# Performance work log

Measured on AMD Instinct MI355X. Metric: run time of the kernel, lower is better.

Reference implementation:

```python
import jax, jax.numpy as jnp
import numpy as np

B, C, T, K = 16, 512, 2048, 64

def setup_inputs() -> dict:
    key = jax.random.key(0)
    k1, k2, k3 = jax.random.split(key, 3)
    v = jax.random.normal(k1, (B, C, T), dtype=jnp.float32)
    # 1x1 Conv1d weights == linear maps over channel dim
    Wk = jax.random.normal(k2, (K, C), dtype=jnp.float32) * 0.02
    bk = jnp.zeros((K,), dtype=jnp.float32)
    Wq = jax.random.normal(k3, (K, C), dtype=jnp.float32) * 0.02
    bq = jnp.zeros((K,), dtype=jnp.float32)
    gamma = jnp.ones((), dtype=jnp.float32)
    return {"v": v, "Wk": Wk, "bk": bk, "Wq": Wq, "bq": bq, "gamma": gamma}

def reference(v, Wk, bk, Wq, bq, gamma):
    # k, q: (B, K, T) via 1x1 conv = channel-wise linear
    k = jnp.einsum('kc,bct->bkt', Wk, v) + bk[None, :, None]
    q = jnp.einsum('kc,bct->bkt', Wq, v) + bq[None, :, None]
    # original: e1[b,d,i,j]=q[b,d,j], e2[b,d,i,j]=k[b,d,i]; sum over d
    # -> s[b,i,j] = sum_d k[b,d,i] * q[b,d,j]  (avoid materializing B,K,T,T)
    s = jnp.einsum('bdi,bdj->bij', k, q)  # (B, T, T)
    a = jax.nn.softmax(s, axis=1)          # softmax over dim=1 (the i axis)
    att = jnp.einsum('bct,btj->bcj', v, a)  # bmm(v, a)
    return v + gamma * att
```

## Files before the change

### kernel.cpp

```cpp
#include <hip/hip_runtime.h>

#define Bc 16
#define Cc 512
#define Tc 2048
#define QT 128
#define KT 128
#define NT 16
#define LTS 66

typedef __attribute__((ext_vector_type(8)))  short short8;
typedef __attribute__((ext_vector_type(4)))  float f32x4;
typedef __attribute__((ext_vector_type(16))) float f32x16;
typedef unsigned short u16;

static __device__ __forceinline__ u16 f2bf(float x) {
  unsigned u = __float_as_uint(x);
  u += 0x7FFF + ((u >> 16) & 1);
  return (u16)(u >> 16);
}

static __device__ __forceinline__ unsigned cvt_pk_bf16(float lo, float hi) {
  unsigned r;
  asm("v_cvt_pk_bf16_f32 %0, %1, %2" : "=v"(r) : "v"(lo), "v"(hi));
  return r;
}

static __device__ __forceinline__ void gload_lds16(const u16* gsrc, u16* ldst) {
  __builtin_amdgcn_global_load_lds(
      (const __attribute__((address_space(1))) unsigned int*)gsrc,
      (__attribute__((address_space(3))) unsigned int*)ldst,
      16, 0, 0);
}

static __device__ __forceinline__ void block_sync_lds() {
  __builtin_amdgcn_sched_barrier(0);
  asm volatile("s_waitcnt lgkmcnt(0)" ::: "memory");
  __builtin_amdgcn_s_barrier();
  __builtin_amdgcn_sched_barrier(0);
}

static __device__ __forceinline__ void block_sync_vm4() {
  __builtin_amdgcn_sched_barrier(0);
  asm volatile("s_waitcnt vmcnt(4) lgkmcnt(0)" ::: "memory");
  __builtin_amdgcn_s_barrier();
  __builtin_amdgcn_sched_barrier(0);
}

__global__ __launch_bounds__(256) void prep_kernel(
    const float* __restrict__ Wk, const float* __restrict__ Wq,
    const float* __restrict__ bk, const float* __restrict__ bq,
    u16* __restrict__ Wbf, float* __restrict__ bkq)
{
  int idx  = blockIdx.x * 256 + threadIdx.x;
  int base = idx * 4;
  if (base < 128 * Cc) {
    int ch = base >> 9;
    int c  = base & (Cc - 1);
    const float* src = (ch < 64) ? (Wk + (size_t)ch * Cc + c)
                                 : (Wq + (size_t)(ch - 64) * Cc + c);
    f32x4 w = *reinterpret_cast<const f32x4*>(src);
    uint2 o;
    o.x = (unsigned)f2bf(w[0]) | ((unsigned)f2bf(w[1]) << 16);
    o.y = (unsigned)f2bf(w[2]) | ((unsigned)f2bf(w[3]) << 16);
    *reinterpret_cast<uint2*>(Wbf + base) = o;
  }
  if (idx < 128) bkq[idx] = (idx < 64) ? bk[idx] : bq[idx - 64];
}

__global__ __launch_bounds__(256) void kqv_kernel(
    const float* __restrict__ v, const u16* __restrict__ Wbf,
    const float* __restrict__ bkq, u16* __restrict__ kq, u16* __restrict__ vbf)
{
  __shared__ u16 LDSt[2][64][LTS];
  const int b   = blockIdx.y;
  const int t0  = blockIdx.x * 64;
  const int tid = threadIdx.x;
  const int lane = tid & 63;
  const int w    = tid >> 6;
  const int l15  = lane & 15;
  const int lg   = lane >> 4;

  f32x4 acc[8];
  #pragma unroll
  for (int mt = 0; mt < 8; ++mt) acc[mt] = f32x4{0.f, 0.f, 0.f, 0.f};

  const float* vb = v + (size_t)b * Cc * Tc + t0;
  float x[16];
  #pragma unroll
  for (int r = 0; r < 16; ++r) x[r] = vb[(size_t)(w * 16 + r) * Tc + lane];

  int buf = 0;
  for (int c0 = 0; c0 < Cc; c0 += 64, buf ^= 1) {
    #pragma unroll
    for (int r = 0; r < 16; ++r) {
      u16 hb = f2bf(x[r]);
      LDSt[buf][lane][w * 16 + r] = hb;
      vbf[((size_t)b * Cc + c0 + w * 16 + r) * Tc + t0 + lane] = hb;
    }
    block_sync_lds();
    if (c0 + 64 < Cc) {
      #pragma unroll
      for (int r = 0; r < 16; ++r)
        x[r] = vb[(size_t)(c0 + 64 + w * 16 + r) * Tc + lane];
    }
    #pragma unroll
    for (int ks = 0; ks < 2; ++ks) {
      short8 bfrag = *reinterpret_cast<const short8*>(&LDSt[buf][w * 16 + l15][ks * 32 + lg * 8]);
      #pragma unroll
      for (int mt = 0; mt < 8; ++mt) {
        short8 afrag = *reinterpret_cast<const short8*>(
            Wbf + (size_t)(mt * 16 + l15) * Cc + c0 + ks * 32 + lg * 8);
        acc[mt] = __builtin_amdgcn_mfma_f32_16x16x32_bf16(afrag, bfrag, acc[mt], 0, 0, 0);
      }
    }
  }
  const int t = t0 + w * 16 + l15;
  u16* op = kq + ((size_t)b * Tc + t) * 128;
  #pragma unroll
  for (int mt = 0; mt < 8; ++mt) {
    int chb = mt * 16 + lg * 4;
    uint2 o;
    o.x = cvt_pk_bf16(acc[mt][0] + bkq[chb + 0], acc[mt][1] + bkq[chb + 1]);
    o.y = cvt_pk_bf16(acc[mt][2] + bkq[chb + 2], acc[mt][3] + bkq[chb + 3]);
    *reinterpret_cast<uint2*>(op + chb) = o;
  }
}

#define VLOAD(VF, KSB, IB)                                                \
  _Pragma("unroll")                                                       \
  for (int ct_ = 0; ct_ < 2; ++ct_)                                       \
    _Pragma("unroll")                                                     \
    for (int kk_ = 0; kk_ < 2; ++kk_)                                     \
      VF[ct_][kk_] = *reinterpret_cast<const short8*>(                    \
          vbase + (size_t)(ct_ * 32 + l31) * Tc + (IB) + ((KSB) + kk_) * 16 + kh * 8);

#define PVSTEP(VF, KSB)                                                   \
  {                                                                       \
    _Pragma("unroll")                                                     \
    for (int kk_ = 0; kk_ < 2; ++kk_) {                                   \
      short8 pf_[4];                                                      \
      _Pragma("unroll")                                                   \
      for (int jt_ = 0; jt_ < 4; ++jt_) {                                 \
        int row_ = jt_ * 32 + l31;                                        \
        int chk_ = ((((KSB) + kk_) * 2 + kh) ^ (row_ & 15)) * 8;          \
        pf_[jt_] = *reinterpret_cast<const short8*>(&P[pb][row_ * 128 + chk_]); \
      }                                                                   \
      _Pragma("unroll")                                                   \
      for (int jt_ = 0; jt_ < 4; ++jt_) {                                 \
        O32[0][jt_] = __builtin_amdgcn_mfma_f32_32x32x16_bf16(VF[0][kk_], pf_[jt_], O32[0][jt_], 0, 0, 0); \
        O32[1][jt_] = __builtin_amdgcn_mfma_f32_32x32x16_bf16(VF[1][kk_], pf_[jt_], O32[1][jt_], 0, 0, 0); \
      }                                                                   \
    }                                                                     \
  }

__global__ __launch_bounds__(512, 2) void attn_kernel(
    const float* __restrict__ v, const u16* __restrict__ vbf,
    const u16* __restrict__ kq, const float* __restrict__ gamma_p,
    float* __restrict__ out)
{
  __shared__ u16 P[2][128 * 128];
  __shared__ u16 Klds[2][128 * 64];
  __shared__ float lsum_lds[QT];
  __shared__ __align__(16) float linv_lds[QT];

  const int L   = blockIdx.x;
  const int lin = (L & 7) * 32 + (L >> 3);
  const int b   = lin >> 4;
  const int j0  = (lin & 15) * QT;
  const int tid = threadIdx.x;
  const int lane = tid & 63;
  const int wid  = tid >> 6;
  const int l15  = lane & 15;
  const int lg   = lane >> 4;
  const int l31  = lane & 31;
  const int kh   = lane >> 5;
  const int c0   = wid * 64;

  const int sc = (lane & 7) ^ ((lane >> 3) & 7);
  const u16* kqb2 = kq + (size_t)b * Tc * 128;
  u16* kst = &Klds[0][0] + wid * 16 * 64;

  short8 qf0, qf1;
  {
    const u16* qp = kq + (size_t)(b * Tc + j0 + wid * 16 + l15) * 128 + 64 + lg * 8;
    qf0 = *reinterpret_cast<const short8*>(qp);
    qf1 = *reinterpret_cast<const short8*>(qp + 32);
  }

  f32x16 O32[2][4];
  #pragma unroll
  for (int a = 0; a < 2; ++a)
    #pragma unroll
    for (int bb = 0; bb < 4; ++bb)
      #pragma unroll
      for (int e = 0; e < 16; ++e) O32[a][bb][e] = 0.f;

  float lsum = 0.f;

  const u16* vbase = vbf + ((size_t)b * Cc + c0) * Tc;
  short8 vfA[2][2], vfB[2][2];

  gload_lds16(kqb2 + (size_t)(wid * 16 + (lane >> 3)) * 128 + sc * 8, kst);
  gload_lds16(kqb2 + (size_t)(wid * 16 + 8 + (lane >> 3)) * 128 + sc * 8, kst + 8 * 64);
  __syncthreads();
  {
    u16* prow = &P[0][(wid * 16 + l15) * 128];
    #pragma unroll
    for (int hg = 0; hg < 2; ++hg) {
      short8 kf[4][2];
      #pragma unroll
      for (int it2 = 0; it2 < 4; ++it2)
        #pragma unroll
        for (int ks = 0; ks < 2; ++ks)
          kf[it2][ks] = *reinterpret_cast<const short8*>(
              &Klds[0][((hg * 4 + it2) * 16 + l15) * 64 + (((ks * 4 + lg) ^ (l15 & 7)) * 8)]);
      f32x4 sacc[4];
      #pragma unroll
      for (int it2 = 0; it2 < 4; ++it2) {
        f32x4 s = f32x4{0.f, 0.f, 0.f, 0.f};
        s = __builtin_amdgcn_mfma_f32_16x16x32_bf16(kf[it2][0], qf0, s, 0, 0, 0);
        s = __builtin_amdgcn_mfma_f32_16x16x32_bf16(kf[it2][1], qf1, s, 0, 0, 0);
        sacc[it2] = s;
      }
      #pragma unroll
      for (int it2 = 0; it2 < 4; ++it2) {
        float p0 = __expf(sacc[it2][0]);
        float p1 = __expf(sacc[it2][1]);
        float p2 = __expf(sacc[it2][2]);
        float p3 = __expf(sacc[it2][3]);
        lsum += (p0 + p1) + (p2 + p3);
        uint2 wv;
        wv.x = cvt_pk_bf16(p0, p1);
        wv.y = cvt_pk_bf16(p2, p3);
        int chk = ((hg * 8 + it2 * 2 + (lg >> 1)) ^ (l15 & 15)) * 8 + (lg & 1) * 4;
        *reinterpret_cast<uint2*>(prow + chk) = wv;
      }
    }
  }
  gload_lds16(kqb2 + (size_t)(KT + wid * 16 + (lane >> 3)) * 128 + sc * 8, kst + 8192);
  gload_lds16(kqb2 + (size_t)(KT + wid * 16 + 8 + (lane >> 3)) * 128 + sc * 8, kst + 8192 + 8 * 64);
  VLOAD(vfA, 0, 0);
  block_sync_vm4();

  int pb = 0;
  for (int i = 0; i < NT; ++i, pb ^= 1) {
    const int i0 = i * KT;
    const bool last = (i + 1 >= NT);

    VLOAD(vfB, 2, i0);

    if (i + 2 < NT) {
      const size_t kb = (size_t)(i0 + 2 * KT);
      gload_lds16(kqb2 + (kb + wid * 16 + (lane >> 3)) * 128 + sc * 8,
                  kst + (i & 1) * 8192);
      gload_lds16(kqb2 + (kb + wid * 16 + 8 + (lane >> 3)) * 128 + sc * 8,
                  kst + (i & 1) * 8192 + 8 * 64);
    }

    if (!last) {
      const u16* kl = &Klds[(i + 1) & 1][0];
      u16* prow = &P[pb ^ 1][(wid * 16 + l15) * 128];
      #pragma unroll
      for (int hg = 0; hg < 2; ++hg) {
        short8 kf[4][2];
        #pragma unroll
        for (int it2 = 0; it2 < 4; ++it2)
          #pragma unroll
          for (int ks = 0; ks < 2; ++ks)
            kf[it2][ks] = *reinterpret_cast<const short8*>(
                &kl[((hg * 4 + it2) * 16 + l15) * 64 + (((ks * 4 + lg) ^ (l15 & 7)) * 8)]);
        f32x4 sacc[4];
        #pragma unroll
        for (int it2 = 0; it2 < 4; ++it2) {
          f32x4 s = f32x4{0.f, 0.f, 0.f, 0.f};
          s = __builtin_amdgcn_mfma_f32_16x16x32_bf16(kf[it2][0], qf0, s, 0, 0, 0);
          s = __builtin_amdgcn_mfma_f32_16x16x32_bf16(kf[it2][1], qf1, s, 0, 0, 0);
          sacc[it2] = s;
        }
        #pragma unroll
        for (int it2 = 0; it2 < 4; ++it2) {
          float p0 = __expf(sacc[it2][0]);
          float p1 = __expf(sacc[it2][1]);
          float p2 = __expf(sacc[it2][2]);
          float p3 = __expf(sacc[it2][3]);
          lsum += (p0 + p1) + (p2 + p3);
          uint2 wv;
          wv.x = cvt_pk_bf16(p0, p1);
          wv.y = cvt_pk_bf16(p2, p3);
          int chk = ((hg * 8 + it2 * 2 + (lg >> 1)) ^ (l15 & 15)) * 8 + (lg & 1) * 4;
          *reinterpret_cast<uint2*>(prow + chk) = wv;
        }
      }
    }

    PVSTEP(vfA, 0);
    VLOAD(vfA, 4, i0);
    PVSTEP(vfB, 2);
    VLOAD(vfB, 6, i0);
    PVSTEP(vfA, 4);
    if (!last) VLOAD(vfA, 0, i0 + KT);
    PVSTEP(vfB, 6);

    if (!last) block_sync_vm4();
  }

  lsum += __shfl_xor(lsum, 16);
  lsum += __shfl_xor(lsum, 32);
  if (lane < 16) lsum_lds[wid * 16 + lane] = lsum;
  __syncthreads();
  const float gamma = *gamma_p;
  if (tid < QT) linv_lds[tid] = gamma / lsum_lds[tid];
  __syncthreads();

  float* ep = reinterpret_cast<float*>(&P[0][0]) + wid * (32 * 36);
  const int rd_row = lane >> 3;
  const int rd_ch  = lane & 7;
  #pragma unroll
  for (int ct = 0; ct < 2; ++ct) {
    #pragma unroll
    for (int jt = 0; jt < 4; ++jt) {
      #pragma unroll
      for (int reg = 0; reg < 16; ++reg) {
        int cl = (reg & 3) + 8 * (reg >> 2) + 4 * kh;
        ep[cl * 36 + l31] = O32[ct][jt][reg];
      }
      asm volatile("s_waitcnt lgkmcnt(0)" ::: "memory");
      __builtin_amdgcn_sched_barrier(0);
      #pragma unroll
      for (int h = 0; h < 4; ++h) {
        const int row = rd_row + 8 * h;
        f32x4 o4 = *reinterpret_cast<const f32x4*>(&ep[row * 36 + rd_ch * 4]);
        const int jg = jt * 32 + rd_ch * 4;
        f32x4 li = *reinterpret_cast<const f32x4*>(&linv_lds[jg]);
        const int c_glob = c0 + ct * 32 + row;
        const float* vr = v + ((size_t)(b * Cc + c_glob)) * Tc + j0 + jg;
        float* orow = out + ((size_t)(b * Cc + c_glob)) * Tc + j0 + jg;
        f32x4 v4 = *reinterpret_cast<const f32x4*>(vr);
        f32x4 o;
        o[0] = v4[0] + li[0] * o4[0];
        o[1] = v4[1] + li[1] * o4[1];
        o[2] = v4[2] + li[2] * o4[2];
        o[3] = v4[3] + li[3] * o4[3];
        *reinterpret_cast<f32x4*>(orow) = o;
      }
      asm volatile("s_waitcnt lgkmcnt(0)" ::: "memory");
      __builtin_amdgcn_sched_barrier(0);
    }
  }
}

extern "C" void kernel_launch(void* const* d_in, const int* in_sizes, int n_in,
                              void* d_out, int out_size, void* d_ws, size_t ws_size,
                              hipStream_t stream) {
  const float* v  = (const float*)d_in[0];
  const float* Wk = (const float*)d_in[1];
  const float* bk = (const float*)d_in[2];
  const float* Wq = (const float*)d_in[3];
  const float* bq = (const float*)d_in[4];
  const float* gm = (const float*)d_in[5];
  float* out = (float*)d_out;

  char* ws = (char*)d_ws;
  u16*   kqb = (u16*)ws;
  u16*   vbf = (u16*)(ws + 8388608);
  u16*   Wbf = (u16*)(ws + 8388608 + 33554432);
  float* bkq = (float*)(ws + 8388608 + 33554432 + 131072);

  prep_kernel<<<dim3(64), dim3(256), 0, stream>>>(Wk, Wq, bk, bq, Wbf, bkq);
  kqv_kernel<<<dim3(Tc / 64, Bc), dim3(256), 0, stream>>>(v, Wbf, bkq, kqb, vbf);
  attn_kernel<<<dim3((Tc / QT) * Bc), dim3(512), 0, stream>>>(v, vbf, kqb, gm, out);
}
```

Before: 157.1 us.

## Stagger S-phase and PV-phase order across wave halves with MFMA priority

Refactors the score/exp phase and the PV accumulation group into macros. Waves 0-3 now run PV first and then the next tile's scores, while waves 4-7 do the reverse, so different waves issue MFMA-heavy and exp/VALU-heavy work at the same time. It also raises wave priority around the PV MFMA steps with s_setprio. The goal is better overlap of MFMA, transcendental and LDS work inside the block, at the cost of possibly different LDS contention and register-scheduling behaviour.

Result: slower. 194.6 us (+23.9%).

```diff
diff --git a/kernel.cpp b/kernel.cpp
--- a/kernel.cpp
+++ b/kernel.cpp
@@ -153,6 +153,62 @@
     }                                                                     \
   }
 
+#define PVGROUP(I0, LAST)                                                 \
+  {                                                                       \
+    __builtin_amdgcn_s_setprio(1);                                        \
+    PVSTEP(vfA, 0);                                                       \
+    __builtin_amdgcn_s_setprio(0);                                        \
+    VLOAD(vfA, 4, (I0));                                                  \
+    __builtin_amdgcn_s_setprio(1);                                        \
+    PVSTEP(vfB, 2);                                                       \
+    __builtin_amdgcn_s_setprio(0);                                        \
+    VLOAD(vfB, 6, (I0));                                                  \
+    __builtin_amdgcn_s_setprio(1);                                        \
+    PVSTEP(vfA, 4);                                                       \
+    __builtin_amdgcn_s_setprio(0);                                        \
+    if (!(LAST)) VLOAD(vfA, 0, (I0) + KT);                                \
+    __builtin_amdgcn_s_setprio(1);                                        \
+    PVSTEP(vfB, 6);                                                       \
+    __builtin_amdgcn_s_setprio(0);                                        \
+  }
+
+#define SPHASE(KL)                                                        \
+  {                                                                       \
+    const u16* kl_ = (KL);                                                \
+    u16* prow_ = &P[pb ^ 1][(wid * 16 + l15) * 128];                      \
+    _Pragma("unroll")                                                     \
+    for (int hg = 0; hg < 2; ++hg) {                                      \
+      short8 kf[4][2];                                                    \
+      _Pragma("unroll")                                                   \
+      for (int it2 = 0; it2 < 4; ++it2)                                   \
+        _Pragma("unroll")                                                 \
+        for (int ks = 0; ks < 2; ++ks)                                    \
+          kf[it2][ks] = *reinterpret_cast<const short8*>(                 \
+              &kl_[((hg * 4 + it2) * 16 + l15) * 64 + (((ks * 4 + lg) ^ (l15 & 7)) * 8)]); \
+      f32x4 sacc[4];                                                      \
+      _Pragma("unroll")                                                   \
+      for (int it2 = 0; it2 < 4; ++it2) {                                 \
+        f32x4 s = f32x4{0.f, 0.f, 0.f, 0.f};                              \
+        s = __builtin_amdgcn_mfma_f32_16x16x32_bf16(kf[it2][0], qf0, s, 0, 0, 0); \
+        s = __builtin_amdgcn_mfma_f32_16x16x32_bf16(kf[it2][1], qf1, s, 0, 0, 0); \
+        sacc[it2] = s;                                                    \
+      }                                                                   \
+      _Pragma("unroll")                                                   \
+      for (int it2 = 0; it2 < 4; ++it2) {                                 \
+        float p0 = __expf(sacc[it2][0]);                                  \
+        float p1 = __expf(sacc[it2][1]);                                  \
+        float p2 = __expf(sacc[it2][2]);                                  \
+        float p3 = __expf(sacc[it2][3]);                                  \
+        lsum += (p0 + p1) + (p2 + p3);                                    \
+        uint2 wv;                                                         \
+        wv.x = cvt_pk_bf16(p0, p1);                                       \
+        wv.y = cvt_pk_bf16(p2, p3);                                       \
+        int chk = ((hg * 8 + it2 * 2 + (lg >> 1)) ^ (l15 & 15)) * 8 + (lg & 1) * 4; \
+        *reinterpret_cast<uint2*>(prow_ + chk) = wv;                      \
+      }                                                                   \
+    }                                                                     \
+  }
+
 __global__ __launch_bounds__(512, 2) void attn_kernel(
     const float* __restrict__ v, const u16* __restrict__ vbf,
     const u16* __restrict__ kq, const float* __restrict__ gamma_p,
@@ -204,38 +260,8 @@
   gload_lds16(kqb2 + (size_t)(wid * 16 + 8 + (lane >> 3)) * 128 + sc * 8, kst + 8 * 64);
   __syncthreads();
   {
-    u16* prow = &P[0][(wid * 16 + l15) * 128];
-    #pragma unroll
-    for (int hg = 0; hg < 2; ++hg) {
-      short8 kf[4][2];
-      #pragma unroll
-      for (int it2 = 0; it2 < 4; ++it2)
-        #pragma unroll
-        for (int ks = 0; ks < 2; ++ks)
-          kf[it2][ks] = *reinterpret_cast<const short8*>(
-              &Klds[0][((hg * 4 + it2) * 16 + l15) * 64 + (((ks * 4 + lg) ^ (l15 & 7)) * 8)]);
-      f32x4 sacc[4];
-      #pragma unroll
-      for (int it2 = 0; it2 < 4; ++it2) {
-        f32x4 s = f32x4{0.f, 0.f, 0.f, 0.f};
-        s = __builtin_amdgcn_mfma_f32_16x16x32_bf16(kf[it2][0], qf0, s, 0, 0, 0);
-        s = __builtin_amdgcn_mfma_f32_16x16x32_bf16(kf[it2][1], qf1, s, 0, 0, 0);
-        sacc[it2] = s;
-      }
-      #pragma unroll
-      for (int it2 = 0; it2 < 4; ++it2) {
-        float p0 = __expf(sacc[it2][0]);
-        float p1 = __expf(sacc[it2][1]);
-        float p2 = __expf(sacc[it2][2]);
-        float p3 = __expf(sacc[it2][3]);
-        lsum += (p0 + p1) + (p2 + p3);
-        uint2 wv;
-        wv.x = cvt_pk_bf16(p0, p1);
-        wv.y = cvt_pk_bf16(p2, p3);
-        int chk = ((hg * 8 + it2 * 2 + (lg >> 1)) ^ (l15 & 15)) * 8 + (lg & 1) * 4;
-        *reinterpret_cast<uint2*>(prow + chk) = wv;
-      }
-    }
+    int pb = 1;
+    SPHASE(&Klds[0][0]);
   }
   gload_lds16(kqb2 + (size_t)(KT + wid * 16 + (lane >> 3)) * 128 + sc * 8, kst + 8192);
   gload_lds16(kqb2 + (size_t)(KT + wid * 16 + 8 + (lane >> 3)) * 128 + sc * 8, kst + 8192 + 8 * 64);
@@ -257,49 +283,13 @@
                   kst + (i & 1) * 8192 + 8 * 64);
     }
 
-    if (!last) {
-      const u16* kl = &Klds[(i + 1) & 1][0];
-      u16* prow = &P[pb ^ 1][(wid * 16 + l15) * 128];
-      #pragma unroll
-      for (int hg = 0; hg < 2; ++hg) {
-        short8 kf[4][2];
-        #pragma unroll
-        for (int it2 = 0; it2 < 4; ++it2)
-          #pragma unroll
-          for (int ks = 0; ks < 2; ++ks)
-            kf[it2][ks] = *reinterpret_cast<const short8*>(
-                &kl[((hg * 4 + it2) * 16 + l15) * 64 + (((ks * 4 + lg) ^ (l15 & 7)) * 8)]);
-        f32x4 sacc[4];
-        #pragma unroll
-        for (int it2 = 0; it2 < 4; ++it2) {
-          f32x4 s = f32x4{0.f, 0.f, 0.f, 0.f};
-          s = __builtin_amdgcn_mfma_f32_16x16x32_bf16(kf[it2][0], qf0, s, 0, 0, 0);
-          s = __builtin_amdgcn_mfma_f32_16x16x32_bf16(kf[it2][1], qf1, s, 0, 0, 0);
-          sacc[it2] = s;
-        }
-        #pragma unroll
-        for (int it2 = 0; it2 < 4; ++it2) {
-          float p0 = __expf(sacc[it2][0]);
-          float p1 = __expf(sacc[it2][1]);
-          float p2 = __expf(sacc[it2][2]);
-          float p3 = __expf(sacc[it2][3]);
-          lsum += (p0 + p1) + (p2 + p3);
-          uint2 wv;
-          wv.x = cvt_pk_bf16(p0, p1);
-          wv.y = cvt_pk_bf16(p2, p3);
-          int chk = ((hg * 8 + it2 * 2 + (lg >> 1)) ^ (l15 & 15)) * 8 + (lg & 1) * 4;
-          *reinterpret_cast<uint2*>(prow + chk) = wv;
-        }
-      }
-    }
-
-    PVSTEP(vfA, 0);
-    VLOAD(vfA, 4, i0);
-    PVSTEP(vfB, 2);
-    VLOAD(vfB, 6, i0);
-    PVSTEP(vfA, 4);
-    if (!last) VLOAD(vfA, 0, i0 + KT);
-    PVSTEP(vfB, 6);
+    if (wid < 4) {
+      PVGROUP(i0, last);
+      if (!last) SPHASE(&Klds[(i + 1) & 1][0]);
+    } else {
+      if (!last) SPHASE(&Klds[(i + 1) & 1][0]);
+      PVGROUP(i0, last);
+    }
 
     if (!last) block_sync_vm4();
   }
```
